# Kernel tuning notes

Measured on AMD Instinct MI355X. Metric: run time of the kernel, lower is better.

The kernel has to match this reference:

```python
import jax, jax.numpy as jnp
import numpy as np

N = 8000          # num_nodes
DEG = 8           # avg out-degree of random road graph
B = 32            # batch size
INPUT_DIM = 2
UNITS = 64        # rnn_units
K = 2             # max_diffusion_step
NUM_SUPPORTS = 2  # dual_random_walk


def _spmm(rows, cols, vals, x):
    # sparse @ dense: y[r] += vals * x[c] for each coo entry (r, c)
    return jax.ops.segment_sum(vals[:, None] * x[cols], rows, num_segments=N)


def _gconv(inputs, state, supports, W, b):
    # Chebyshev-style diffusion conv, faithful to GCONV.forward layout
    Bsz = inputs.shape[0]
    x = jnp.concatenate([inputs.reshape(Bsz, N, -1), state.reshape(Bsz, N, -1)], axis=2)
    F = x.shape[2]                                   # input_dim + units
    x0 = jnp.transpose(x, (1, 2, 0)).reshape(N, F * Bsz)
    xs = [x0]
    for rows, cols, vals in supports:
        x1 = _spmm(rows, cols, vals, x0)
        xs.append(x1)
        xk2, xk1 = x0, x1
        for _ in range(2, K + 1):
            x2 = 2.0 * _spmm(rows, cols, vals, xk1) - xk2
            xs.append(x2)
            xk2, xk1 = xk1, x2
    M = len(xs)                                      # num_matrices = 2*K+1
    xc = jnp.stack(xs).reshape(M, N, F, Bsz)
    xc = jnp.transpose(xc, (3, 1, 2, 0)).reshape(Bsz * N, F * M)
    out = xc @ W + b
    return out.reshape(Bsz, N * W.shape[1])


def setup_inputs() -> dict:
    rng = np.random.default_rng(0)
    rows = np.repeat(np.arange(N, dtype=np.int32), DEG)
    cols = rng.integers(0, N, size=N * DEG).astype(np.int32)
    vals = rng.uniform(0.5, 1.5, size=N * DEG).astype(np.float32)
    # random-walk normalization: rw(A) = D^-1 A ; supports are rw(A).T and rw(A.T).T
    rsum = np.zeros(N, np.float32); np.add.at(rsum, rows, vals)
    csum = np.zeros(N, np.float32); np.add.at(csum, cols, vals)
    rinv = np.where(rsum > 0, 1.0 / np.maximum(rsum, 1e-12), 0.0).astype(np.float32)
    cinv = np.where(csum > 0, 1.0 / np.maximum(csum, 1e-12), 0.0).astype(np.float32)
    # support0 = (D^-1 A)^T: entry (cols[i], rows[i]) = vals[i] * rinv[rows[i]]
    s0_rows, s0_cols, s0_vals = cols, rows, (vals * rinv[rows]).astype(np.float32)
    # support1 = (D_T^-1 A^T)^T: entry (rows[i], cols[i]) = vals[i] * cinv[cols[i]]
    s1_rows, s1_cols, s1_vals = rows, cols, (vals * cinv[cols]).astype(np.float32)

    key = jax.random.key(0)
    k1, k2, k3, k4 = jax.random.split(key, 4)
    F = INPUT_DIM + UNITS
    M = NUM_SUPPORTS * K + 1
    xavier = lambda k, shape: jax.random.normal(k, shape, jnp.float32) * np.float32(np.sqrt(2.0 / (shape[0] + shape[1])))
    W_ru = xavier(k1, (F * M, 2 * UNITS))
    b_ru = jnp.ones((2 * UNITS,), jnp.float32)    # bias_start=1.0
    W_c = xavier(k2, (F * M, UNITS))
    b_c = jnp.zeros((UNITS,), jnp.float32)        # bias_start=0.0
    inputs = jax.random.normal(k3, (B, N * INPUT_DIM), jnp.float32)
    hx = jax.random.normal(k4, (B, N * UNITS), jnp.float32)
    return {
        "inputs": inputs, "hx": hx,
        "W_ru": W_ru, "b_ru": b_ru, "W_c": W_c, "b_c": b_c,
        "s0_rows": jnp.asarray(s0_rows), "s0_cols": jnp.asarray(s0_cols), "s0_vals": jnp.asarray(s0_vals),
        "s1_rows": jnp.asarray(s1_rows), "s1_cols": jnp.asarray(s1_cols), "s1_vals": jnp.asarray(s1_vals),
    }


def reference(inputs, hx, W_ru, b_ru, W_c, b_c,
              s0_rows, s0_cols, s0_vals, s1_rows, s1_cols, s1_vals):
    supports = [(s0_rows, s0_cols, s0_vals), (s1_rows, s1_cols, s1_vals)]
    value = jax.nn.sigmoid(_gconv(inputs, hx, supports, W_ru, b_ru))
    value = value.reshape(-1, N, 2 * UNITS)
    r = value[..., :UNITS].reshape(-1, N * UNITS)
    u = value[..., UNITS:].reshape(-1, N * UNITS)
    c = jnp.tanh(_gconv(inputs, r * hx, supports, W_c, b_c))
    return u * hx + (1.0 - u) * c
```

## Files before the change

### kernel.cpp

```cpp
#include <hip/hip_runtime.h>
#include <stdint.h>

typedef unsigned short u16;
typedef unsigned int   u32;

typedef __attribute__((ext_vector_type(8))) short bf16x8;
typedef __attribute__((ext_vector_type(4))) float f32x4;

#define NNODES 8000
#define BSZ    32
#define UNITS  64
#define EDG    64000
#define ROWCH  288
#define ROWU16 2304
#define KLIN   480
#define HXROW  512000
#define INROW  16000
#define NROW   18432000

__device__ __forceinline__ u32 f2bf(float f){
    u32 u = __float_as_uint(f);
    return (u + 0x7FFFu + ((u >> 16) & 1u)) >> 16;
}
__device__ __forceinline__ float bfu(u16 s){ return __uint_as_float(((u32)s) << 16); }
__device__ __forceinline__ float lo16(u32 u){ return __uint_as_float(u << 16); }
__device__ __forceinline__ float hi16(u32 u){ return __uint_as_float(u & 0xFFFF0000u); }
__device__ __forceinline__ float sigm(float x){ return 1.f / (1.f + __expf(-x)); }

__global__ void hist_k(const int* __restrict__ rows, int* __restrict__ counts){
    int e = blockIdx.x * 256 + threadIdx.x;
    if (e < EDG) atomicAdd(&counts[rows[e]], 1);
}

__global__ __launch_bounds__(256) void scan_k(const int* __restrict__ counts,
                                              int* __restrict__ row_ptr,
                                              int* __restrict__ cursor){
    __shared__ int part[256];
    int t = threadIdx.x;
    int s = 0;
    for (int i = 0; i < 32; ++i){ int r = t*32 + i; if (r < NNODES) s += counts[r]; }
    part[t] = s;
    __syncthreads();
    if (t == 0){
        int run = 0;
        for (int i = 0; i < 256; ++i){ int v = part[i]; part[i] = run; run += v; }
    }
    __syncthreads();
    int run = part[t];
    for (int i = 0; i < 32; ++i){
        int r = t*32 + i;
        if (r < NNODES){ row_ptr[r] = run; cursor[r] = run; run += counts[r]; }
    }
    if (t == 255) row_ptr[NNODES] = run;
}

__global__ void scatter_k(const int* __restrict__ rows, const int* __restrict__ cols,
                          const float* __restrict__ vals, int* __restrict__ cursor,
                          int* __restrict__ cs, float* __restrict__ vs){
    int e = blockIdx.x * 256 + threadIdx.x;
    if (e < EDG){
        int r = rows[e];
        int slot = atomicAdd(&cursor[r], 1);
        cs[slot] = cols[e];
        vs[slot] = vals[e];
    }
}

__global__ void prep_w_k(const float* __restrict__ W_ru, const float* __restrict__ W_c,
                         u16* __restrict__ Wt_ru, u16* __restrict__ Wt_c){
    int id = blockIdx.x * 256 + threadIdx.x;
    if (id < 128*KLIN){
        int c = id / KLIN, kl = id % KLIN;
        int m = kl / 96, fp = kl - m*96;
        u16 v = 0;
        if (fp < 66) v = (u16)f2bf(W_ru[(fp*5 + m)*128 + c]);
        Wt_ru[id] = v;
    }
    int id2 = id - 128*KLIN;
    if (id2 >= 0 && id2 < 64*KLIN){
        int c = id2 / KLIN, kl = id2 % KLIN;
        int m = kl / 96, fp = kl - m*96;
        u16 v = 0;
        if (fp < 66) v = (u16)f2bf(W_c[(fp*5 + m)*64 + c]);
        Wt_c[id2] = v;
    }
}

__global__ __launch_bounds__(256) void build_x0_k(const float* __restrict__ inputs,
                                                  const float* __restrict__ hx,
                                                  u16* __restrict__ X0){
    __shared__ float sl[32*72];
    int n = blockIdx.x, t = threadIdx.x;
    #pragma unroll
    for (int i = 0; i < 8; ++i){
        int idx = t + i*256;
        int b = idx >> 6, f = idx & 63;
        sl[b*72 + 2 + f] = hx[b*HXROW + n*64 + f];
    }
    if (t < 64){
        int b = t >> 1, d = t & 1;
        sl[b*72 + d] = inputs[b*INROW + n*2 + d];
    }
    if (t < 192){
        int b = t / 6, k = t - b*6;
        sl[b*72 + 66 + k] = 0.f;
    }
    __syncthreads();
    #pragma unroll
    for (int i = 0; i < 2; ++i){
        int j = t + i*256;
        if (j < ROWCH){
            int b = j & 31, s = j >> 5;
            const float* p = &sl[b*72 + s*8];
            uint4 o;
            o.x = f2bf(p[0]) | (f2bf(p[1]) << 16);
            o.y = f2bf(p[2]) | (f2bf(p[3]) << 16);
            o.z = f2bf(p[4]) | (f2bf(p[5]) << 16);
            o.w = f2bf(p[6]) | (f2bf(p[7]) << 16);
            ((uint4*)X0)[n*ROWCH + j] = o;
        }
    }
}

__device__ __forceinline__ void acc8(float* a, uint4 q, float v){
    a[0] += v*lo16(q.x); a[1] += v*hi16(q.x);
    a[2] += v*lo16(q.y); a[3] += v*hi16(q.y);
    a[4] += v*lo16(q.z); a[5] += v*hi16(q.z);
    a[6] += v*lo16(q.w); a[7] += v*hi16(q.w);
}
__device__ __forceinline__ uint4 pack8(const float* a){
    uint4 o;
    o.x = f2bf(a[0]) | (f2bf(a[1]) << 16);
    o.y = f2bf(a[2]) | (f2bf(a[3]) << 16);
    o.z = f2bf(a[4]) | (f2bf(a[5]) << 16);
    o.w = f2bf(a[6]) | (f2bf(a[7]) << 16);
    return o;
}

__global__ __launch_bounds__(288) void diff1_k(const u16* __restrict__ X0,
                                               u16* __restrict__ X1a, u16* __restrict__ X1b,
                                               const int* __restrict__ rp,
                                               const int* __restrict__ c0, const float* __restrict__ v0,
                                               const int* __restrict__ c1, const float* __restrict__ v1){
    int t = threadIdx.x;
    if (t >= ROWCH) return;
    int n = blockIdx.x;
    const uint4* xb = (const uint4*)X0;
    float a[8] = {0,0,0,0,0,0,0,0};
    float d[8] = {0,0,0,0,0,0,0,0};
    {
        uint4 q[8]; float vv[8];
        #pragma unroll
        for (int i = 0; i < 8; ++i){
            int c = c1[n*8 + i]; vv[i] = v1[n*8 + i];
            q[i] = xb[(size_t)c*ROWCH + t];
        }
        #pragma unroll
        for (int i = 0; i < 8; ++i) acc8(d, q[i], vv[i]);
    }
    int e = rp[n], end = rp[n+1];
    for (; e + 8 <= end; e += 8){
        uint4 q[8]; float vv[8];
        #pragma unroll
        for (int i = 0; i < 8; ++i){
            int c = c0[e+i]; vv[i] = v0[e+i];
            q[i] = xb[(size_t)c*ROWCH + t];
        }
        #pragma unroll
        for (int i = 0; i < 8; ++i) acc8(a, q[i], vv[i]);
    }
    for (; e < end; ++e){
        int c = c0[e]; float v = v0[e];
        acc8(a, xb[(size_t)c*ROWCH + t], v);
    }
    ((uint4*)X1a)[(size_t)n*ROWCH + t] = pack8(a);
    ((uint4*)X1b)[(size_t)n*ROWCH + t] = pack8(d);
}

__global__ __launch_bounds__(288) void diff2_k(const u16* __restrict__ X0,
                                               const u16* __restrict__ X1a, const u16* __restrict__ X1b,
                                               u16* __restrict__ X2a, u16* __restrict__ X2b,
                                               const int* __restrict__ rp,
                                               const int* __restrict__ c0, const float* __restrict__ v0,
                                               const int* __restrict__ c1, const float* __restrict__ v1){
    int t = threadIdx.x;
    if (t >= ROWCH) return;
    int n = blockIdx.x;
    const uint4* xa = (const uint4*)X1a;
    const uint4* xbb = (const uint4*)X1b;
    uint4 pv = ((const uint4*)X0)[(size_t)n*ROWCH + t];
    float a[8] = {0,0,0,0,0,0,0,0};
    float d[8] = {0,0,0,0,0,0,0,0};
    {
        uint4 q[8]; float vv[8];
        #pragma unroll
        for (int i = 0; i < 8; ++i){
            int c = c1[n*8 + i]; vv[i] = v1[n*8 + i];
            q[i] = xbb[(size_t)c*ROWCH + t];
        }
        #pragma unroll
        for (int i = 0; i < 8; ++i) acc8(d, q[i], vv[i]);
    }
    int e = rp[n], end = rp[n+1];
    for (; e + 8 <= end; e += 8){
        uint4 q[8]; float vv[8];
        #pragma unroll
        for (int i = 0; i < 8; ++i){
            int c = c0[e+i]; vv[i] = v0[e+i];
            q[i] = xa[(size_t)c*ROWCH + t];
        }
        #pragma unroll
        for (int i = 0; i < 8; ++i) acc8(a, q[i], vv[i]);
    }
    for (; e < end; ++e){
        int c = c0[e]; float v = v0[e];
        acc8(a, xa[(size_t)c*ROWCH + t], v);
    }
    float p[8] = { lo16(pv.x), hi16(pv.x), lo16(pv.y), hi16(pv.y),
                   lo16(pv.z), hi16(pv.z), lo16(pv.w), hi16(pv.w) };
    #pragma unroll
    for (int i = 0; i < 8; ++i){ a[i] = 2.f*a[i] - p[i]; d[i] = 2.f*d[i] - p[i]; }
    ((uint4*)X2a)[(size_t)n*ROWCH + t] = pack8(a);
    ((uint4*)X2b)[(size_t)n*ROWCH + t] = pack8(d);
}

__global__ __launch_bounds__(256) void gemm_ru_k(
        const u16* X0, const u16* __restrict__ X1a, const u16* __restrict__ X2a,
        const u16* __restrict__ X1b, const u16* __restrict__ X2b,
        const u16* __restrict__ Wt,
        const float* __restrict__ b_ru,
        u16* __restrict__ U, u16* X0st){
    const int t = threadIdx.x;
    const int lane = t & 63, w = t >> 6;
    const int node = blockIdx.x*4 + w;
    const int cIn = lane & 15, q = lane >> 4;
    const size_t noff = (size_t)node * ROWU16;

    const u16* xp[5] = { X0 + noff, X1a + noff, X2a + noff, X1b + noff, X2b + noff };

    f32x4 acc[2][8];
    const f32x4 z4 = {0.f,0.f,0.f,0.f};
    #pragma unroll
    for (int rt = 0; rt < 2; ++rt)
        #pragma unroll
        for (int ct = 0; ct < 8; ++ct) acc[rt][ct] = z4;

    bf16x8 ca0, ca1, cb[8], na0, na1, nb[8];
    ca0 = *(const bf16x8*)&xp[0][(size_t)((0*4 + q)*32 + 0*16 + cIn)*8];
    ca1 = *(const bf16x8*)&xp[0][(size_t)((0*4 + q)*32 + 1*16 + cIn)*8];
    #pragma unroll
    for (int ct = 0; ct < 8; ++ct)
        cb[ct] = *(const bf16x8*)&Wt[(ct*16 + cIn)*KLIN + 0*32 + q*8];

    #pragma unroll
    for (int st = 0; st < 15; ++st){
        if (st < 14){
            const int m2 = (st+1)/3, sub2 = (st+1) - m2*3;
            na0 = *(const bf16x8*)&xp[m2][(size_t)((sub2*4 + q)*32 + 0*16 + cIn)*8];
            na1 = *(const bf16x8*)&xp[m2][(size_t)((sub2*4 + q)*32 + 1*16 + cIn)*8];
            #pragma unroll
            for (int ct = 0; ct < 8; ++ct)
                nb[ct] = *(const bf16x8*)&Wt[(ct*16 + cIn)*KLIN + (st+1)*32 + q*8];
        }
        #pragma unroll
        for (int ct = 0; ct < 8; ++ct){
            acc[0][ct] = __builtin_amdgcn_mfma_f32_16x16x32_bf16(ca0, cb[ct], acc[0][ct], 0,0,0);
            acc[1][ct] = __builtin_amdgcn_mfma_f32_16x16x32_bf16(ca1, cb[ct], acc[1][ct], 0,0,0);
        }
        ca0 = na0; ca1 = na1;
        #pragma unroll
        for (int ct = 0; ct < 8; ++ct) cb[ct] = nb[ct];
    }

    #pragma unroll
    for (int ct = 0; ct < 8; ++ct){
        int col = ct*16 + cIn;
        float bias = b_ru[col];
        #pragma unroll
        for (int rt = 0; rt < 2; ++rt){
            int b0 = rt*16 + q*4;
            f32x4 d = acc[rt][ct];
            if (ct < 4){
                int fp = 2 + col;
                int s = fp >> 3, off = fp & 7;
                #pragma unroll
                for (int i = 0; i < 4; ++i){
                    size_t idx = noff + (size_t)(s*32 + b0 + i)*8 + off;
                    float h = bfu(X0st[idx]);
                    float rg = sigm(d[i] + bias);
                    X0st[idx] = (u16)f2bf(rg * h);
                }
            } else {
                uint2 pk;
                float v0 = sigm(d[0] + bias), v1 = sigm(d[1] + bias);
                float v2 = sigm(d[2] + bias), v3 = sigm(d[3] + bias);
                pk.x = f2bf(v0) | (f2bf(v1) << 16);
                pk.y = f2bf(v2) | (f2bf(v3) << 16);
                *(uint2*)&U[(size_t)node*2048 + (col - 64)*32 + b0] = pk;
            }
        }
    }
}

__global__ __launch_bounds__(256) void gemm_c_k(
        const u16* __restrict__ X0, const u16* __restrict__ X1a, const u16* __restrict__ X2a,
        const u16* __restrict__ X1b, const u16* __restrict__ X2b,
        const u16* __restrict__ Wt,
        const float* __restrict__ b_c, const float* __restrict__ hx,
        const u16* __restrict__ U, float* __restrict__ out){
    const int t = threadIdx.x;
    const int lane = t & 63, w = t >> 6;
    const int node = blockIdx.x*4 + w;
    const int cIn = lane & 15, q = lane >> 4;
    const size_t noff = (size_t)node * ROWU16;

    const u16* xp[5] = { X0 + noff, X1a + noff, X2a + noff, X1b + noff, X2b + noff };

    f32x4 acc[2][4];
    const f32x4 z4 = {0.f,0.f,0.f,0.f};
    #pragma unroll
    for (int rt = 0; rt < 2; ++rt)
        #pragma unroll
        for (int ct = 0; ct < 4; ++ct) acc[rt][ct] = z4;

    bf16x8 ca0, ca1, cb[4], na0, na1, nb[4];
    ca0 = *(const bf16x8*)&xp[0][(size_t)((0*4 + q)*32 + 0*16 + cIn)*8];
    ca1 = *(const bf16x8*)&xp[0][(size_t)((0*4 + q)*32 + 1*16 + cIn)*8];
    #pragma unroll
    for (int ct = 0; ct < 4; ++ct)
        cb[ct] = *(const bf16x8*)&Wt[(ct*16 + cIn)*KLIN + 0*32 + q*8];

    #pragma unroll
    for (int st = 0; st < 15; ++st){
        if (st < 14){
            const int m2 = (st+1)/3, sub2 = (st+1) - m2*3;
            na0 = *(const bf16x8*)&xp[m2][(size_t)((sub2*4 + q)*32 + 0*16 + cIn)*8];
            na1 = *(const bf16x8*)&xp[m2][(size_t)((sub2*4 + q)*32 + 1*16 + cIn)*8];
            #pragma unroll
            for (int ct = 0; ct < 4; ++ct)
                nb[ct] = *(const bf16x8*)&Wt[(ct*16 + cIn)*KLIN + (st+1)*32 + q*8];
        }
        #pragma unroll
        for (int ct = 0; ct < 4; ++ct){
            acc[0][ct] = __builtin_amdgcn_mfma_f32_16x16x32_bf16(ca0, cb[ct], acc[0][ct], 0,0,0);
            acc[1][ct] = __builtin_amdgcn_mfma_f32_16x16x32_bf16(ca1, cb[ct], acc[1][ct], 0,0,0);
        }
        ca0 = na0; ca1 = na1;
        #pragma unroll
        for (int ct = 0; ct < 4; ++ct) cb[ct] = nb[ct];
    }

    #pragma unroll
    for (int ct = 0; ct < 4; ++ct){
        int col = ct*16 + cIn;
        float bias = b_c[col];
        #pragma unroll
        for (int rt = 0; rt < 2; ++rt){
            int b0 = rt*16 + q*4;
            f32x4 d = acc[rt][ct];
            uint2 up = *(const uint2*)&U[(size_t)node*2048 + col*32 + b0];
            float uu[4] = { lo16(up.x), hi16(up.x), lo16(up.y), hi16(up.y) };
            #pragma unroll
            for (int i = 0; i < 4; ++i){
                float c = tanhf(d[i] + bias);
                size_t gi = (size_t)(b0 + i)*HXROW + node*64 + col;
                float h = hx[gi];
                out[gi] = uu[i]*h + (1.f - uu[i])*c;
            }
        }
    }
}

extern "C" void kernel_launch(void* const* d_in, const int* in_sizes, int n_in,
                              void* d_out, int out_size, void* d_ws, size_t ws_size,
                              hipStream_t stream){
    const float* inputs = (const float*)d_in[0];
    const float* hx     = (const float*)d_in[1];
    const float* W_ru   = (const float*)d_in[2];
    const float* b_ru   = (const float*)d_in[3];
    const float* W_c    = (const float*)d_in[4];
    const float* b_c    = (const float*)d_in[5];
    const int*   s0r    = (const int*)d_in[6];
    const int*   s0c    = (const int*)d_in[7];
    const float* s0v    = (const float*)d_in[8];
    const int*   s1c    = (const int*)d_in[10];
    const float* s1v    = (const float*)d_in[11];
    float* out = (float*)d_out;

    char* ws = (char*)d_ws;
    size_t off = 0;
    auto alloc = [&](size_t bytes) -> char* {
        char* p = ws + off;
        off += (bytes + 255) & ~(size_t)255;
        return p;
    };
    const size_t XBYTES = (size_t)NROW*2 + 2048;
    u16* X0   = (u16*)alloc(XBYTES);
    u16* X1a  = (u16*)alloc(XBYTES);
    u16* X2a  = (u16*)alloc(XBYTES);
    u16* X1b  = (u16*)alloc(XBYTES);
    u16* X2b  = (u16*)alloc(XBYTES);
    u16* U    = (u16*)alloc((size_t)NNODES*2048*2);
    u16* WtRU = (u16*)alloc((size_t)128*KLIN*2);
    u16* WtC  = (u16*)alloc((size_t)64*KLIN*2);
    int* counts  = (int*)alloc((size_t)NNODES*4);
    int* row_ptr = (int*)alloc((size_t)(NNODES+1)*4);
    int* cursor  = (int*)alloc((size_t)NNODES*4);
    int*   cols_s = (int*)alloc((size_t)EDG*4);
    float* vals_s = (float*)alloc((size_t)EDG*4);
    (void)ws_size; (void)in_sizes; (void)n_in; (void)out_size;

    hipMemsetAsync(counts, 0, (size_t)NNODES*4, stream);
    hist_k<<<250, 256, 0, stream>>>(s0r, counts);
    scan_k<<<1, 256, 0, stream>>>(counts, row_ptr, cursor);
    scatter_k<<<250, 256, 0, stream>>>(s0r, s0c, s0v, cursor, cols_s, vals_s);

    prep_w_k<<<360, 256, 0, stream>>>(W_ru, W_c, WtRU, WtC);
    build_x0_k<<<NNODES, 256, 0, stream>>>(inputs, hx, X0);

    diff1_k<<<NNODES, 288, 0, stream>>>(X0, X1a, X1b, row_ptr, cols_s, vals_s, s1c, s1v);
    diff2_k<<<NNODES, 288, 0, stream>>>(X0, X1a, X1b, X2a, X2b, row_ptr, cols_s, vals_s, s1c, s1v);

    gemm_ru_k<<<NNODES/4, 256, 0, stream>>>(X0, X1a, X2a, X1b, X2b, WtRU, b_ru, U, X0);

    diff1_k<<<NNODES, 288, 0, stream>>>(X0, X1a, X1b, row_ptr, cols_s, vals_s, s1c, s1v);
    diff2_k<<<NNODES, 288, 0, stream>>>(X0, X1a, X1b, X2a, X2b, row_ptr, cols_s, vals_s, s1c, s1v);

    gemm_c_k<<<NNODES/4, 256, 0, stream>>>(X0, X1a, X2a, X1b, X2b, WtC, b_c, hx, U, out);
}
```

Before: 720.7 us.

## Interleave diffusion matrices per node and drop zero padding from GEMM K dimension

```diff
diff --git a/kernel.cpp b/kernel.cpp
--- a/kernel.cpp
+++ b/kernel.cpp
@@ -8,15 +8,14 @@
 typedef __attribute__((ext_vector_type(4))) float f32x4;
 
 #define NNODES 8000
-#define BSZ    32
-#define UNITS  64
 #define EDG    64000
-#define ROWCH  288
-#define ROWU16 2304
-#define KLIN   480
+#define MATCH  288
+#define NODECH 1440
+#define NODEU16 11520
+#define KLIN   384
+#define NSTEPS 12
 #define HXROW  512000
 #define INROW  16000
-#define NROW   18432000
 
 __device__ __forceinline__ u32 f2bf(float f){
     u32 u = __float_as_uint(f);
@@ -71,53 +70,53 @@
     int id = blockIdx.x * 256 + threadIdx.x;
     if (id < 128*KLIN){
         int c = id / KLIN, kl = id % KLIN;
-        int m = kl / 96, fp = kl - m*96;
+        int m = kl / 72, fp = kl - m*72;
         u16 v = 0;
-        if (fp < 66) v = (u16)f2bf(W_ru[(fp*5 + m)*128 + c]);
+        if (m < 5 && fp < 66) v = (u16)f2bf(W_ru[(fp*5 + m)*128 + c]);
         Wt_ru[id] = v;
     }
     int id2 = id - 128*KLIN;
     if (id2 >= 0 && id2 < 64*KLIN){
         int c = id2 / KLIN, kl = id2 % KLIN;
-        int m = kl / 96, fp = kl - m*96;
+        int m = kl / 72, fp = kl - m*72;
         u16 v = 0;
-        if (fp < 66) v = (u16)f2bf(W_c[(fp*5 + m)*64 + c]);
+        if (m < 5 && fp < 66) v = (u16)f2bf(W_c[(fp*5 + m)*64 + c]);
         Wt_c[id2] = v;
     }
 }
 
 __global__ __launch_bounds__(256) void build_x0_k(const float* __restrict__ inputs,
                                                   const float* __restrict__ hx,
-                                                  u16* __restrict__ X0){
-    __shared__ float sl[32*72];
+                                                  u16* __restrict__ Xu){
+    __shared__ float sl[32*73];
     int n = blockIdx.x, t = threadIdx.x;
     #pragma unroll
     for (int i = 0; i < 8; ++i){
         int idx = t + i*256;
         int b = idx >> 6, f = idx & 63;
-        sl[b*72 + 2 + f] = hx[b*HXROW + n*64 + f];
+        sl[b*73 + 2 + f] = hx[b*HXROW + n*64 + f];
     }
     if (t < 64){
         int b = t >> 1, d = t & 1;
-        sl[b*72 + d] = inputs[b*INROW + n*2 + d];
+        sl[b*73 + d] = inputs[b*INROW + n*2 + d];
     }
     if (t < 192){
         int b = t / 6, k = t - b*6;
-        sl[b*72 + 66 + k] = 0.f;
+        sl[b*73 + 66 + k] = 0.f;
     }
     __syncthreads();
     #pragma unroll
     for (int i = 0; i < 2; ++i){
         int j = t + i*256;
-        if (j < ROWCH){
+        if (j < MATCH){
             int b = j & 31, s = j >> 5;
-            const float* p = &sl[b*72 + s*8];
+            const float* p = &sl[b*73 + s*8];
             uint4 o;
             o.x = f2bf(p[0]) | (f2bf(p[1]) << 16);
             o.y = f2bf(p[2]) | (f2bf(p[3]) << 16);
             o.z = f2bf(p[4]) | (f2bf(p[5]) << 16);
             o.w = f2bf(p[6]) | (f2bf(p[7]) << 16);
-            ((uint4*)X0)[n*ROWCH + j] = o;
+            ((uint4*)Xu)[(size_t)n*NODECH + j] = o;
         }
     }
 }
@@ -137,15 +136,15 @@
     return o;
 }
 
-__global__ __launch_bounds__(288) void diff1_k(const u16* __restrict__ X0,
-                                               u16* __restrict__ X1a, u16* __restrict__ X1b,
+__global__ __launch_bounds__(576) void diff1_k(u16* Xu,
                                                const int* __restrict__ rp,
                                                const int* __restrict__ c0, const float* __restrict__ v0,
                                                const int* __restrict__ c1, const float* __restrict__ v1){
     int t = threadIdx.x;
-    if (t >= ROWCH) return;
-    int n = blockIdx.x;
-    const uint4* xb = (const uint4*)X0;
+    int half = (t >= MATCH) ? 1 : 0;
+    int tt = t - half*MATCH;
+    int n = blockIdx.x*2 + half;
+    const uint4* xb = (const uint4*)Xu;
     float a[8] = {0,0,0,0,0,0,0,0};
     float d[8] = {0,0,0,0,0,0,0,0};
     {
@@ -153,7 +152,7 @@
         #pragma unroll
         for (int i = 0; i < 8; ++i){
             int c = c1[n*8 + i]; vv[i] = v1[n*8 + i];
-            q[i] = xb[(size_t)c*ROWCH + t];
+            q[i] = xb[(size_t)c*NODECH + tt];
         }
         #pragma unroll
         for (int i = 0; i < 8; ++i) acc8(d, q[i], vv[i]);
@@ -164,31 +163,29 @@
         #pragma unroll
         for (int i = 0; i < 8; ++i){
             int c = c0[e+i]; vv[i] = v0[e+i];
-            q[i] = xb[(size_t)c*ROWCH + t];
+            q[i] = xb[(size_t)c*NODECH + tt];
         }
         #pragma unroll
         for (int i = 0; i < 8; ++i) acc8(a, q[i], vv[i]);
     }
     for (; e < end; ++e){
         int c = c0[e]; float v = v0[e];
-        acc8(a, xb[(size_t)c*ROWCH + t], v);
-    }
-    ((uint4*)X1a)[(size_t)n*ROWCH + t] = pack8(a);
-    ((uint4*)X1b)[(size_t)n*ROWCH + t] = pack8(d);
-}
-
-__global__ __launch_bounds__(288) void diff2_k(const u16* __restrict__ X0,
-                                               const u16* __restrict__ X1a, const u16* __restrict__ X1b,
-                                               u16* __restrict__ X2a, u16* __restrict__ X2b,
+        acc8(a, xb[(size_t)c*NODECH + tt], v);
+    }
+    ((uint4*)Xu)[(size_t)n*NODECH + 1*MATCH + tt] = pack8(a);
+    ((uint4*)Xu)[(size_t)n*NODECH + 3*MATCH + tt] = pack8(d);
+}
+
+__global__ __launch_bounds__(576) void diff2_k(u16* Xu,
                                                const int* __restrict__ rp,
                                                const int* __restrict__ c0, const float* __restrict__ v0,
                                                const int* __restrict__ c1, const float* __restrict__ v1){
     int t = threadIdx.x;
-    if (t >= ROWCH) return;
-    int n = blockIdx.x;
-    const uint4* xa = (const uint4*)X1a;
-    const uint4* xbb = (const uint4*)X1b;
-    uint4 pv = ((const uint4*)X0)[(size_t)n*ROWCH + t];
+    int half = (t >= MATCH) ? 1 : 0;
+    int tt = t - half*MATCH;
+    int n = blockIdx.x*2 + half;
+    const uint4* xb = (const uint4*)Xu;
+    uint4 pv = xb[(size_t)n*NODECH + tt];
     float a[8] = {0,0,0,0,0,0,0,0};
     float d[8] = {0,0,0,0,0,0,0,0};
     {
@@ -196,7 +193,7 @@
         #pragma unroll
         for (int i = 0; i < 8; ++i){
             int c = c1[n*8 + i]; vv[i] = v1[n*8 + i];
-            q[i] = xbb[(size_t)c*ROWCH + t];
+            q[i] = xb[(size_t)c*NODECH + 3*MATCH + tt];
         }
         #pragma unroll
         for (int i = 0; i < 8; ++i) acc8(d, q[i], vv[i]);
@@ -207,26 +204,25 @@
         #pragma unroll
         for (int i = 0; i < 8; ++i){
             int c = c0[e+i]; vv[i] = v0[e+i];
-            q[i] = xa[(size_t)c*ROWCH + t];
+            q[i] = xb[(size_t)c*NODECH + 1*MATCH + tt];
         }
         #pragma unroll
         for (int i = 0; i < 8; ++i) acc8(a, q[i], vv[i]);
     }
     for (; e < end; ++e){
         int c = c0[e]; float v = v0[e];
-        acc8(a, xa[(size_t)c*ROWCH + t], v);
+        acc8(a, xb[(size_t)c*NODECH + 1*MATCH + tt], v);
     }
     float p[8] = { lo16(pv.x), hi16(pv.x), lo16(pv.y), hi16(pv.y),
                    lo16(pv.z), hi16(pv.z), lo16(pv.w), hi16(pv.w) };
     #pragma unroll
     for (int i = 0; i < 8; ++i){ a[i] = 2.f*a[i] - p[i]; d[i] = 2.f*d[i] - p[i]; }
-    ((uint4*)X2a)[(size_t)n*ROWCH + t] = pack8(a);
-    ((uint4*)X2b)[(size_t)n*ROWCH + t] = pack8(d);
-}
-
-__global__ __launch_bounds__(256) void gemm_ru_k(
-        const u16* X0, const u16* __restrict__ X1a, const u16* __restrict__ X2a,
-        const u16* __restrict__ X1b, const u16* __restrict__ X2b,
+    ((uint4*)Xu)[(size_t)n*NODECH + 2*MATCH + tt] = pack8(a);
+    ((uint4*)Xu)[(size_t)n*NODECH + 4*MATCH + tt] = pack8(d);
+}
+
+__global__ __launch_bounds__(256, 4) void gemm_ru_k(
+        const u16* Xu,
         const u16* __restrict__ Wt,
         const float* __restrict__ b_ru,
         u16* __restrict__ U, u16* X0st){
@@ -234,9 +230,8 @@
     const int lane = t & 63, w = t >> 6;
     const int node = blockIdx.x*4 + w;
     const int cIn = lane & 15, q = lane >> 4;
-    const size_t noff = (size_t)node * ROWU16;
-
-    const u16* xp[5] = { X0 + noff, X1a + noff, X2a + noff, X1b + noff, X2b + noff };
+    const size_t noff = (size_t)node * NODEU16;
+    const u16* Xn = Xu + noff;
 
     f32x4 acc[2][8];
     const f32x4 z4 = {0.f,0.f,0.f,0.f};
@@ -245,31 +240,38 @@
         #pragma unroll
         for (int ct = 0; ct < 8; ++ct) acc[rt][ct] = z4;
 
-    bf16x8 ca0, ca1, cb[8], na0, na1, nb[8];
-    ca0 = *(const bf16x8*)&xp[0][(size_t)((0*4 + q)*32 + 0*16 + cIn)*8];
-    ca1 = *(const bf16x8*)&xp[0][(size_t)((0*4 + q)*32 + 1*16 + cIn)*8];
+    bf16x8 A0[2], A1[2], cb[8], nb[8];
+    A0[0] = *(const bf16x8*)&Xn[(size_t)((0*4 + q)*32 +  0 + cIn)*8];
+    A1[0] = *(const bf16x8*)&Xn[(size_t)((0*4 + q)*32 + 16 + cIn)*8];
+    A0[1] = *(const bf16x8*)&Xn[(size_t)((1*4 + q)*32 +  0 + cIn)*8];
+    A1[1] = *(const bf16x8*)&Xn[(size_t)((1*4 + q)*32 + 16 + cIn)*8];
     #pragma unroll
     for (int ct = 0; ct < 8; ++ct)
-        cb[ct] = *(const bf16x8*)&Wt[(ct*16 + cIn)*KLIN + 0*32 + q*8];
-
-    #pragma unroll
-    for (int st = 0; st < 15; ++st){
-        if (st < 14){
-            const int m2 = (st+1)/3, sub2 = (st+1) - m2*3;
-            na0 = *(const bf16x8*)&xp[m2][(size_t)((sub2*4 + q)*32 + 0*16 + cIn)*8];
-            na1 = *(const bf16x8*)&xp[m2][(size_t)((sub2*4 + q)*32 + 1*16 + cIn)*8];
+        cb[ct] = *(const bf16x8*)&Wt[(size_t)(ct*16 + cIn)*KLIN + q*8];
+
+    #pragma unroll
+    for (int st = 0; st < NSTEPS; ++st){
+        const int cur = st & 1;
+        if (st + 1 < NSTEPS){
             #pragma unroll
             for (int ct = 0; ct < 8; ++ct)
-                nb[ct] = *(const bf16x8*)&Wt[(ct*16 + cIn)*KLIN + (st+1)*32 + q*8];
+                nb[ct] = *(const bf16x8*)&Wt[(size_t)(ct*16 + cIn)*KLIN + (st+1)*32 + q*8];
+        }
+        bf16x8 p0, p1;
+        if (st + 2 < NSTEPS){
+            p0 = *(const bf16x8*)&Xn[(size_t)(((st+2)*4 + q)*32 +  0 + cIn)*8];
+            p1 = *(const bf16x8*)&Xn[(size_t)(((st+2)*4 + q)*32 + 16 + cIn)*8];
         }
         #pragma unroll
         for (int ct = 0; ct < 8; ++ct){
-            acc[0][ct] = __builtin_amdgcn_mfma_f32_16x16x32_bf16(ca0, cb[ct], acc[0][ct], 0,0,0);
-            acc[1][ct] = __builtin_amdgcn_mfma_f32_16x16x32_bf16(ca1, cb[ct], acc[1][ct], 0,0,0);
-        }
-        ca0 = na0; ca1 = na1;
-        #pragma unroll
-        for (int ct = 0; ct < 8; ++ct) cb[ct] = nb[ct];
+            acc[0][ct] = __builtin_amdgcn_mfma_f32_16x16x32_bf16(A0[cur], cb[ct], acc[0][ct], 0,0,0);
+            acc[1][ct] = __builtin_amdgcn_mfma_f32_16x16x32_bf16(A1[cur], cb[ct], acc[1][ct], 0,0,0);
+        }
+        if (st + 2 < NSTEPS){ A0[cur] = p0; A1[cur] = p1; }
+        if (st + 1 < NSTEPS){
+            #pragma unroll
+            for (int ct = 0; ct < 8; ++ct) cb[ct] = nb[ct];
+        }
     }
 
     #pragma unroll
@@ -302,9 +304,8 @@
     }
 }
 
-__global__ __launch_bounds__(256) void gemm_c_k(
-        const u16* __restrict__ X0, const u16* __restrict__ X1a, const u16* __restrict__ X2a,
-        const u16* __restrict__ X1b, const u16* __restrict__ X2b,
+__global__ __launch_bounds__(256, 4) void gemm_c_k(
+        const u16* __restrict__ Xu,
         const u16* __restrict__ Wt,
         const float* __restrict__ b_c, const float* __restrict__ hx,
         const u16* __restrict__ U, float* __restrict__ out){
@@ -312,9 +313,8 @@
     const int lane = t & 63, w = t >> 6;
     const int node = blockIdx.x*4 + w;
     const int cIn = lane & 15, q = lane >> 4;
-    const size_t noff = (size_t)node * ROWU16;
-
-    const u16* xp[5] = { X0 + noff, X1a + noff, X2a + noff, X1b + noff, X2b + noff };
+    const size_t noff = (size_t)node * NODEU16;
+    const u16* Xn = Xu + noff;
 
     f32x4 acc[2][4];
     const f32x4 z4 = {0.f,0.f,0.f,0.f};
@@ -323,31 +323,38 @@
         #pragma unroll
         for (int ct = 0; ct < 4; ++ct) acc[rt][ct] = z4;
 
-    bf16x8 ca0, ca1, cb[4], na0, na1, nb[4];
-    ca0 = *(const bf16x8*)&xp[0][(size_t)((0*4 + q)*32 + 0*16 + cIn)*8];
-    ca1 = *(const bf16x8*)&xp[0][(size_t)((0*4 + q)*32 + 1*16 + cIn)*8];
+    bf16x8 A0[2], A1[2], cb[4], nb[4];
+    A0[0] = *(const bf16x8*)&Xn[(size_t)((0*4 + q)*32 +  0 + cIn)*8];
+    A1[0] = *(const bf16x8*)&Xn[(size_t)((0*4 + q)*32 + 16 + cIn)*8];
+    A0[1] = *(const bf16x8*)&Xn[(size_t)((1*4 + q)*32 +  0 + cIn)*8];
+    A1[1] = *(const bf16x8*)&Xn[(size_t)((1*4 + q)*32 + 16 + cIn)*8];
     #pragma unroll
     for (int ct = 0; ct < 4; ++ct)
-        cb[ct] = *(const bf16x8*)&Wt[(ct*16 + cIn)*KLIN + 0*32 + q*8];
-
-    #pragma unroll
-    for (int st = 0; st < 15; ++st){
-        if (st < 14){
-            const int m2 = (st+1)/3, sub2 = (st+1) - m2*3;
-            na0 = *(const bf16x8*)&xp[m2][(size_t)((sub2*4 + q)*32 + 0*16 + cIn)*8];
-            na1 = *(const bf16x8*)&xp[m2][(size_t)((sub2*4 + q)*32 + 1*16 + cIn)*8];
+        cb[ct] = *(const bf16x8*)&Wt[(size_t)(ct*16 + cIn)*KLIN + q*8];
+
+    #pragma unroll
+    for (int st = 0; st < NSTEPS; ++st){
+        const int cur = st & 1;
+        if (st + 1 < NSTEPS){
             #pragma unroll
             for (int ct = 0; ct < 4; ++ct)
-                nb[ct] = *(const bf16x8*)&Wt[(ct*16 + cIn)*KLIN + (st+1)*32 + q*8];
+                nb[ct] = *(const bf16x8*)&Wt[(size_t)(ct*16 + cIn)*KLIN + (st+1)*32 + q*8];
+        }
+        bf16x8 p0, p1;
+        if (st + 2 < NSTEPS){
+            p0 = *(const bf16x8*)&Xn[(size_t)(((st+2)*4 + q)*32 +  0 + cIn)*8];
+            p1 = *(const bf16x8*)&Xn[(size_t)(((st+2)*4 + q)*32 + 16 + cIn)*8];
         }
         #pragma unroll
         for (int ct = 0; ct < 4; ++ct){
-            acc[0][ct] = __builtin_amdgcn_mfma_f32_16x16x32_bf16(ca0, cb[ct], acc[0][ct], 0,0,0);
-            acc[1][ct] = __builtin_amdgcn_mfma_f32_16x16x32_bf16(ca1, cb[ct], acc[1][ct], 0,0,0);
-        }
-        ca0 = na0; ca1 = na1;
-        #pragma unroll
-        for (int ct = 0; ct < 4; ++ct) cb[ct] = nb[ct];
+            acc[0][ct] = __builtin_amdgcn_mfma_f32_16x16x32_bf16(A0[cur], cb[ct], acc[0][ct], 0,0,0);
+            acc[1][ct] = __builtin_amdgcn_mfma_f32_16x16x32_bf16(A1[cur], cb[ct], acc[1][ct], 0,0,0);
+        }
+        if (st + 2 < NSTEPS){ A0[cur] = p0; A1[cur] = p1; }
+        if (st + 1 < NSTEPS){
+            #pragma unroll
+            for (int ct = 0; ct < 4; ++ct) cb[ct] = nb[ct];
+        }
     }
 
     #pragma unroll
@@ -394,12 +401,8 @@
         off += (bytes + 255) & ~(size_t)255;
         return p;
     };
-    const size_t XBYTES = (size_t)NROW*2 + 2048;
-    u16* X0   = (u16*)alloc(XBYTES);
-    u16* X1a  = (u16*)alloc(XBYTES);
-    u16* X2a  = (u16*)alloc(XBYTES);
-    u16* X1b  = (u16*)alloc(XBYTES);
-    u16* X2b  = (u16*)alloc(XBYTES);
+    const size_t XU_BYTES = (size_t)NNODES * NODEU16 * 2;
+    u16* Xu   = (u16*)alloc(XU_BYTES + 4096);
     u16* U    = (u16*)alloc((size_t)NNODES*2048*2);
     u16* WtRU = (u16*)alloc((size_t)128*KLIN*2);
     u16* WtC  = (u16*)alloc((size_t)64*KLIN*2);
@@ -411,20 +414,21 @@
     (void)ws_size; (void)in_sizes; (void)n_in; (void)out_size;
 
     hipMemsetAsync(counts, 0, (size_t)NNODES*4, stream);
+    hipMemsetAsync((char*)Xu + XU_BYTES, 0, 4096, stream);
     hist_k<<<250, 256, 0, stream>>>(s0r, counts);
     scan_k<<<1, 256, 0, stream>>>(counts, row_ptr, cursor);
     scatter_k<<<250, 256, 0, stream>>>(s0r, s0c, s0v, cursor, cols_s, vals_s);
 
-    prep_w_k<<<360, 256, 0, stream>>>(W_ru, W_c, WtRU, WtC);
-    build_x0_k<<<NNODES, 256, 0, stream>>>(inputs, hx, X0);
-
-    diff1_k<<<NNODES, 288, 0, stream>>>(X0, X1a, X1b, row_ptr, cols_s, vals_s, s1c, s1v);
-    diff2_k<<<NNODES, 288, 0, stream>>>(X0, X1a, X1b, X2a, X2b, row_ptr, cols_s, vals_s, s1c, s1v);
-
-    gemm_ru_k<<<NNODES/4, 256, 0, stream>>>(X0, X1a, X2a, X1b, X2b, WtRU, b_ru, U, X0);
-
-    diff1_k<<<NNODES, 288, 0, stream>>>(X0, X1a, X1b, row_ptr, cols_s, vals_s, s1c, s1v);
-    diff2_k<<<NNODES, 288, 0, stream>>>(X0, X1a, X1b, X2a, X2b, row_ptr, cols_s, vals_s, s1c, s1v);
-
-    gemm_c_k<<<NNODES/4, 256, 0, stream>>>(X0, X1a, X2a, X1b, X2b, WtC, b_c, hx, U, out);
-}
+    prep_w_k<<<288, 256, 0, stream>>>(W_ru, W_c, WtRU, WtC);
+    build_x0_k<<<NNODES, 256, 0, stream>>>(inputs, hx, Xu);
+
+    diff1_k<<<NNODES/2, 576, 0, stream>>>(Xu, row_ptr, cols_s, vals_s, s1c, s1v);
+    diff2_k<<<NNODES/2, 576, 0, stream>>>(Xu, row_ptr, cols_s, vals_s, s1c, s1v);
+
+    gemm_ru_k<<<NNODES/4, 256, 0, stream>>>(Xu, WtRU, b_ru, U, Xu);
+
+    diff1_k<<<NNODES/2, 576, 0, stream>>>(Xu, row_ptr, cols_s, vals_s, s1c, s1v);
+    diff2_k<<<NNODES/2, 576, 0, stream>>>(Xu, row_ptr, cols_s, vals_s, s1c, s1v);
+
+    gemm_c_k<<<NNODES/4, 256, 0, stream>>>(Xu, WtC, b_c, hx, U, out);
+}
```

Result: slower. 823.3 us (+14.2%).

## Stage GEMM weights through LDS via async global-to-LDS double buffering

Applied to the files above, without the earlier changes.

```diff
diff --git a/kernel.cpp b/kernel.cpp
--- a/kernel.cpp
+++ b/kernel.cpp
@@ -17,6 +17,7 @@
 #define HXROW  512000
 #define INROW  16000
 #define NROW   18432000
+#define NSTEPS 15
 
 __device__ __forceinline__ u32 f2bf(float f){
     u32 u = __float_as_uint(f);
@@ -26,6 +27,10 @@
 __device__ __forceinline__ float lo16(u32 u){ return __uint_as_float(u << 16); }
 __device__ __forceinline__ float hi16(u32 u){ return __uint_as_float(u & 0xFFFF0000u); }
 __device__ __forceinline__ float sigm(float x){ return 1.f / (1.f + __expf(-x)); }
+
+#define GLDS(gsrc, ldst) \
+    __builtin_amdgcn_global_load_lds((const __attribute__((address_space(1))) void*)(gsrc), \
+                                     (__attribute__((address_space(3))) void*)(ldst), 16, 0, 0)
 
 __global__ void hist_k(const int* __restrict__ rows, int* __restrict__ counts){
     int e = blockIdx.x * 256 + threadIdx.x;
@@ -70,18 +75,26 @@
                          u16* __restrict__ Wt_ru, u16* __restrict__ Wt_c){
     int id = blockIdx.x * 256 + threadIdx.x;
     if (id < 128*KLIN){
-        int c = id / KLIN, kl = id % KLIN;
+        int j = id & 7;
+        int cell = id >> 3;
+        int col = cell & 127;
+        int sq = cell >> 7;
+        int kl = sq*8 + j;
         int m = kl / 96, fp = kl - m*96;
         u16 v = 0;
-        if (fp < 66) v = (u16)f2bf(W_ru[(fp*5 + m)*128 + c]);
+        if (fp < 66) v = (u16)f2bf(W_ru[(fp*5 + m)*128 + col]);
         Wt_ru[id] = v;
     }
     int id2 = id - 128*KLIN;
     if (id2 >= 0 && id2 < 64*KLIN){
-        int c = id2 / KLIN, kl = id2 % KLIN;
+        int j = id2 & 7;
+        int cell = id2 >> 3;
+        int col = cell & 63;
+        int sq = cell >> 6;
+        int kl = sq*8 + j;
         int m = kl / 96, fp = kl - m*96;
         u16 v = 0;
-        if (fp < 66) v = (u16)f2bf(W_c[(fp*5 + m)*64 + c]);
+        if (fp < 66) v = (u16)f2bf(W_c[(fp*5 + m)*64 + col]);
         Wt_c[id2] = v;
     }
 }
@@ -227,9 +240,10 @@
 __global__ __launch_bounds__(256) void gemm_ru_k(
         const u16* X0, const u16* __restrict__ X1a, const u16* __restrict__ X2a,
         const u16* __restrict__ X1b, const u16* __restrict__ X2b,
-        const u16* __restrict__ Wt,
+        const u16* __restrict__ WtS,
         const float* __restrict__ b_ru,
         u16* __restrict__ U, u16* X0st){
+    __shared__ u16 Bs[2][4096];
     const int t = threadIdx.x;
     const int lane = t & 63, w = t >> 6;
     const int node = blockIdx.x*4 + w;
@@ -245,31 +259,39 @@
         #pragma unroll
         for (int ct = 0; ct < 8; ++ct) acc[rt][ct] = z4;
 
-    bf16x8 ca0, ca1, cb[8], na0, na1, nb[8];
-    ca0 = *(const bf16x8*)&xp[0][(size_t)((0*4 + q)*32 + 0*16 + cIn)*8];
-    ca1 = *(const bf16x8*)&xp[0][(size_t)((0*4 + q)*32 + 1*16 + cIn)*8];
-    #pragma unroll
-    for (int ct = 0; ct < 8; ++ct)
-        cb[ct] = *(const bf16x8*)&Wt[(ct*16 + cIn)*KLIN + 0*32 + q*8];
-
-    #pragma unroll
-    for (int st = 0; st < 15; ++st){
-        if (st < 14){
-            const int m2 = (st+1)/3, sub2 = (st+1) - m2*3;
-            na0 = *(const bf16x8*)&xp[m2][(size_t)((sub2*4 + q)*32 + 0*16 + cIn)*8];
-            na1 = *(const bf16x8*)&xp[m2][(size_t)((sub2*4 + q)*32 + 1*16 + cIn)*8];
-            #pragma unroll
-            for (int ct = 0; ct < 8; ++ct)
-                nb[ct] = *(const bf16x8*)&Wt[(ct*16 + cIn)*KLIN + (st+1)*32 + q*8];
-        }
+    {
+        const u16* src = WtS + t*8;
+        GLDS(src,        &Bs[0][w*512]);
+        GLDS(src + 2048, &Bs[0][2048 + w*512]);
+    }
+    bf16x8 A0 = *(const bf16x8*)&xp[0][(size_t)(q*32 + cIn)*8];
+    bf16x8 A1 = *(const bf16x8*)&xp[0][(size_t)(q*32 + 16 + cIn)*8];
+    __syncthreads();
+
+    int cur = 0;
+    #pragma unroll
+    for (int st = 0; st < NSTEPS; ++st){
+        bf16x8 p0, p1;
+        if (st + 1 < NSTEPS){
+            const u16* src = WtS + (size_t)(st+1)*4096 + t*8;
+            GLDS(src,        &Bs[cur^1][w*512]);
+            GLDS(src + 2048, &Bs[cur^1][2048 + w*512]);
+            const int m2 = (st+1)/3, s2 = (st+1) - m2*3;
+            p0 = *(const bf16x8*)&xp[m2][(size_t)((s2*4 + q)*32 + cIn)*8];
+            p1 = *(const bf16x8*)&xp[m2][(size_t)((s2*4 + q)*32 + 16 + cIn)*8];
+        }
+        bf16x8 cb[8];
+        #pragma unroll
+        for (int ct = 0; ct < 8; ++ct)
+            cb[ct] = *(const bf16x8*)&Bs[cur][(q*128 + ct*16 + cIn)*8];
         #pragma unroll
         for (int ct = 0; ct < 8; ++ct){
-            acc[0][ct] = __builtin_amdgcn_mfma_f32_16x16x32_bf16(ca0, cb[ct], acc[0][ct], 0,0,0);
-            acc[1][ct] = __builtin_amdgcn_mfma_f32_16x16x32_bf16(ca1, cb[ct], acc[1][ct], 0,0,0);
-        }
-        ca0 = na0; ca1 = na1;
-        #pragma unroll
-        for (int ct = 0; ct < 8; ++ct) cb[ct] = nb[ct];
+            acc[0][ct] = __builtin_amdgcn_mfma_f32_16x16x32_bf16(A0, cb[ct], acc[0][ct], 0,0,0);
+            acc[1][ct] = __builtin_amdgcn_mfma_f32_16x16x32_bf16(A1, cb[ct], acc[1][ct], 0,0,0);
+        }
+        __syncthreads();
+        if (st + 1 < NSTEPS){ A0 = p0; A1 = p1; }
+        cur ^= 1;
     }
 
     #pragma unroll
@@ -305,9 +327,10 @@
 __global__ __launch_bounds__(256) void gemm_c_k(
         const u16* __restrict__ X0, const u16* __restrict__ X1a, const u16* __restrict__ X2a,
         const u16* __restrict__ X1b, const u16* __restrict__ X2b,
-        const u16* __restrict__ Wt,
+        const u16* __restrict__ WtS,
         const float* __restrict__ b_c, const float* __restrict__ hx,
         const u16* __restrict__ U, float* __restrict__ out){
+    __shared__ u16 Bs[2][2048];
     const int t = threadIdx.x;
     const int lane = t & 63, w = t >> 6;
     const int node = blockIdx.x*4 + w;
@@ -323,31 +346,37 @@
         #pragma unroll
         for (int ct = 0; ct < 4; ++ct) acc[rt][ct] = z4;
 
-    bf16x8 ca0, ca1, cb[4], na0, na1, nb[4];
-    ca0 = *(const bf16x8*)&xp[0][(size_t)((0*4 + q)*32 + 0*16 + cIn)*8];
-    ca1 = *(const bf16x8*)&xp[0][(size_t)((0*4 + q)*32 + 1*16 + cIn)*8];
-    #pragma unroll
-    for (int ct = 0; ct < 4; ++ct)
-        cb[ct] = *(const bf16x8*)&Wt[(ct*16 + cIn)*KLIN + 0*32 + q*8];
-
-    #pragma unroll
-    for (int st = 0; st < 15; ++st){
-        if (st < 14){
-            const int m2 = (st+1)/3, sub2 = (st+1) - m2*3;
-            na0 = *(const bf16x8*)&xp[m2][(size_t)((sub2*4 + q)*32 + 0*16 + cIn)*8];
-            na1 = *(const bf16x8*)&xp[m2][(size_t)((sub2*4 + q)*32 + 1*16 + cIn)*8];
-            #pragma unroll
-            for (int ct = 0; ct < 4; ++ct)
-                nb[ct] = *(const bf16x8*)&Wt[(ct*16 + cIn)*KLIN + (st+1)*32 + q*8];
-        }
+    {
+        const u16* src = WtS + t*8;
+        GLDS(src, &Bs[0][w*512]);
+    }
+    bf16x8 A0 = *(const bf16x8*)&xp[0][(size_t)(q*32 + cIn)*8];
+    bf16x8 A1 = *(const bf16x8*)&xp[0][(size_t)(q*32 + 16 + cIn)*8];
+    __syncthreads();
+
+    int cur = 0;
+    #pragma unroll
+    for (int st = 0; st < NSTEPS; ++st){
+        bf16x8 p0, p1;
+        if (st + 1 < NSTEPS){
+            const u16* src = WtS + (size_t)(st+1)*2048 + t*8;
+            GLDS(src, &Bs[cur^1][w*512]);
+            const int m2 = (st+1)/3, s2 = (st+1) - m2*3;
+            p0 = *(const bf16x8*)&xp[m2][(size_t)((s2*4 + q)*32 + cIn)*8];
+            p1 = *(const bf16x8*)&xp[m2][(size_t)((s2*4 + q)*32 + 16 + cIn)*8];
+        }
+        bf16x8 cb[4];
+        #pragma unroll
+        for (int ct = 0; ct < 4; ++ct)
+            cb[ct] = *(const bf16x8*)&Bs[cur][(q*64 + ct*16 + cIn)*8];
         #pragma unroll
         for (int ct = 0; ct < 4; ++ct){
-            acc[0][ct] = __builtin_amdgcn_mfma_f32_16x16x32_bf16(ca0, cb[ct], acc[0][ct], 0,0,0);
-            acc[1][ct] = __builtin_amdgcn_mfma_f32_16x16x32_bf16(ca1, cb[ct], acc[1][ct], 0,0,0);
-        }
-        ca0 = na0; ca1 = na1;
-        #pragma unroll
-        for (int ct = 0; ct < 4; ++ct) cb[ct] = nb[ct];
+            acc[0][ct] = __builtin_amdgcn_mfma_f32_16x16x32_bf16(A0, cb[ct], acc[0][ct], 0,0,0);
+            acc[1][ct] = __builtin_amdgcn_mfma_f32_16x16x32_bf16(A1, cb[ct], acc[1][ct], 0,0,0);
+        }
+        __syncthreads();
+        if (st + 1 < NSTEPS){ A0 = p0; A1 = p1; }
+        cur ^= 1;
     }
 
     #pragma unroll
```

Measured after the change: 671.4 us. -6.8%, faster.
